# Kernel tuning notes

Hardware: AMD Instinct MI355X
Metric: run time of the kernel (lower is better)

Reference implementation:

```python
import jax, jax.numpy as jnp
import numpy as np

B, S, HID = 2, 2048, 2048
N_HEADS = 16
HEAD_DIM = HID // N_HEADS  # 128
ROPE_THETA = 10000.0
MAX_SEQ = 4096


def _rope_cache(position_ids, head_dim, theta=ROPE_THETA, max_seq=MAX_SEQ):
    # standard RoPE cache: cos/sin of shape [B, S, head_dim//2]
    half = head_dim // 2
    inv_freq = 1.0 / theta ** (jnp.arange(half, dtype=jnp.float32) / half)
    t = jnp.arange(max_seq, dtype=jnp.float32)
    freqs = jnp.outer(t, inv_freq)                      # [max_seq, half]
    pos = jnp.clip(position_ids, 0, max_seq - 1)
    return jnp.cos(freqs)[pos], jnp.sin(freqs)[pos]     # [B, S, half]


def _apply_rope(q, k, cos, sin):
    # q,k: [B, H, S, D]; cos/sin: [B, S, D/2] -> [B, 1, S, D/2]
    cos = cos[:, None, :, :]
    sin = sin[:, None, :, :]
    q1, q2 = jnp.split(q, 2, axis=-1)
    k1, k2 = jnp.split(k, 2, axis=-1)
    q_rot = jnp.concatenate([q1 * cos - q2 * sin, q2 * cos + q1 * sin], axis=-1)
    k_rot = jnp.concatenate([k1 * cos - k2 * sin, k2 * cos + k1 * sin], axis=-1)
    return q_rot, k_rot


def setup_inputs() -> dict:
    key = jax.random.key(0)
    ks = jax.random.split(key, 6)
    hidden_states = jax.random.normal(ks[0], (B, S, HID), dtype=jnp.float32)
    # additive causal mask, broadcastable over batch and heads
    causal = jnp.tril(jnp.ones((S, S), dtype=bool))
    attention_mask = jnp.where(causal, 0.0, -1e9).astype(jnp.float32)[None, None]
    position_ids = jnp.broadcast_to(jnp.arange(S, dtype=jnp.int32)[None, :], (B, S))
    scale = 0.02
    Wq = jax.random.normal(ks[1], (HID, N_HEADS * HEAD_DIM), dtype=jnp.float32) * scale
    Wk = jax.random.normal(ks[2], (HID, N_HEADS * HEAD_DIM), dtype=jnp.float32) * scale
    Wv = jax.random.normal(ks[3], (HID, N_HEADS * HEAD_DIM), dtype=jnp.float32) * scale
    Wo = jax.random.normal(ks[4], (N_HEADS * HEAD_DIM, HID), dtype=jnp.float32) * scale
    zeros = jnp.zeros((HID,), dtype=jnp.float32)
    return {
        "hidden_states": hidden_states,
        "attention_mask": attention_mask,
        "position_ids": position_ids,
        "Wq": Wq, "bq": zeros,
        "Wk": Wk, "bk": zeros,
        "Wv": Wv, "bv": zeros,
        "Wo": Wo, "bo": zeros,
    }


def reference(hidden_states, attention_mask, position_ids,
              Wq, bq, Wk, bk, Wv, bv, Wo, bo):
    b, s, _ = hidden_states.shape
    q = (hidden_states @ Wq + bq).reshape(b, s, N_HEADS, HEAD_DIM).transpose(0, 2, 1, 3)
    k = (hidden_states @ Wk + bk).reshape(b, s, N_HEADS, HEAD_DIM).transpose(0, 2, 1, 3)
    v = (hidden_states @ Wv + bv).reshape(b, s, N_HEADS, HEAD_DIM).transpose(0, 2, 1, 3)

    cos, sin = _rope_cache(position_ids, HEAD_DIM)
    q, k = _apply_rope(q, k, cos, sin)

    scores = jnp.einsum("bhqd,bhkd->bhqk", q, k) / jnp.sqrt(jnp.float32(HEAD_DIM))
    scores = scores + attention_mask
    weights = jax.nn.softmax(scores, axis=-1)
    attn = jnp.einsum("bhqk,bhkd->bhqd", weights, v)  # [B,H,S,D]
    attn = attn.transpose(0, 2, 1, 3).reshape(b, s, N_HEADS * HEAD_DIM)
    return attn @ Wo + bo
```

## Files before the change

kernel.cpp:

```cpp
#include <hip/hip_runtime.h>
#include <hip/hip_bf16.h>

typedef __bf16 bf16;
typedef bf16 bf16x4 __attribute__((ext_vector_type(4)));
typedef bf16 bf16x8 __attribute__((ext_vector_type(8)));
typedef float f32x4 __attribute__((ext_vector_type(4)));

#define B_ 2
#define S_ 2048
#define HID_ 2048
#define NH_ 16
#define HD_ 128
#define M_TOT (B_ * S_)
#define RSCALE 0.08838834764831845f
#define LN10000_OVER_64 0.14391156f

#define OFF_XB   0ull
#define OFF_WQT  (OFF_XB  + (size_t)M_TOT*HID_*2)
#define OFF_WKT  (OFF_WQT + (size_t)HID_*HID_*2)
#define OFF_WVT  (OFF_WKT + (size_t)HID_*HID_*2)
#define OFF_WOT  (OFF_WVT + (size_t)HID_*HID_*2)
#define OFF_QB   (OFF_WOT + (size_t)HID_*HID_*2)
#define OFF_KB   (OFF_QB  + (size_t)M_TOT*HID_*2)
#define OFF_VTB  (OFF_KB  + (size_t)M_TOT*HID_*2)
#define OFF_AB   (OFF_VTB + (size_t)M_TOT*HID_*2)

__device__ __forceinline__ void gload16(const bf16* g, bf16* l) {
    typedef const __attribute__((address_space(1))) unsigned int gu32;
    typedef __attribute__((address_space(3))) unsigned int lu32;
    __builtin_amdgcn_global_load_lds((gu32*)g, (lu32*)l, 16, 0, 0);
}

__global__ __launch_bounds__(256) void cvt_x(const float* __restrict__ x,
                                             bf16* __restrict__ o) {
    size_t i = ((size_t)blockIdx.x * 256 + threadIdx.x) * 4;
    float4 v = *(const float4*)(x + i);
    bf16x4 r; r[0] = (bf16)v.x; r[1] = (bf16)v.y; r[2] = (bf16)v.z; r[3] = (bf16)v.w;
    *(bf16x4*)(o + i) = r;
}

__global__ __launch_bounds__(256) void trans_w(const float* w0, const float* w1,
                                               const float* w2, const float* w3,
                                               bf16* o0, bf16* o1, bf16* o2, bf16* o3) {
    const float* W; bf16* O;
    switch (blockIdx.z) {
        case 0: W = w0; O = o0; break;
        case 1: W = w1; O = o1; break;
        case 2: W = w2; O = o2; break;
        default: W = w3; O = o3; break;
    }
    __shared__ float t[64][65];
    int tid = threadIdx.x;
    int nt0 = blockIdx.x * 64, kt0 = blockIdx.y * 64;
    #pragma unroll
    for (int p = 0; p < 4; ++p) {
        int r = p * 16 + (tid >> 4);
        int c = (tid & 15) * 4;
        float4 v = *(const float4*)(W + (size_t)(kt0 + r) * HID_ + nt0 + c);
        t[r][c + 0] = v.x; t[r][c + 1] = v.y; t[r][c + 2] = v.z; t[r][c + 3] = v.w;
    }
    __syncthreads();
    #pragma unroll
    for (int p = 0; p < 4; ++p) {
        int rr = p * 16 + (tid >> 4);
        int cc = (tid & 15) * 4;
        bf16x4 v;
        v[0] = (bf16)t[cc + 0][rr]; v[1] = (bf16)t[cc + 1][rr];
        v[2] = (bf16)t[cc + 2][rr]; v[3] = (bf16)t[cc + 3][rr];
        *(bf16x4*)(O + (size_t)(nt0 + rr) * HID_ + kt0 + cc) = v;
    }
}

__global__ __launch_bounds__(256) void gemm_qkv(const bf16* __restrict__ A,
                                                const bf16* __restrict__ Wt3,
                                                const float* __restrict__ bq,
                                                const float* __restrict__ bk,
                                                const float* __restrict__ bv,
                                                const int* __restrict__ pos_ids,
                                                bf16* __restrict__ out3) {
    __shared__ bf16 Al[128][64];
    __shared__ bf16 Bl[128][64];
    const int tid = threadIdx.x;
    const int l = tid & 63, w = tid >> 6;
    const int ln = l & 15, lg = l >> 4;
    const int bm = blockIdx.y;
    const int sel = blockIdx.x >> 4, bnn = blockIdx.x & 15;
    const bf16* Bt = Wt3 + (size_t)sel * HID_ * HID_ + (size_t)bnn * 128 * HID_;
    const float* bias = sel == 0 ? bq : (sel == 1 ? bk : bv);
    const int swz = (ln & 7) * 8;

    f32x4 acc[2][8] = {};

    for (int k0 = 0; k0 < HID_; k0 += 64) {
        __syncthreads();
        #pragma unroll
        for (int j = 0; j < 4; ++j) {
            int r0 = w * 32 + j * 8;
            int r = r0 + (l >> 3);
            int c = (((l & 7) ^ ((l >> 3) & 7))) * 8;
            gload16(A  + (size_t)(bm * 128 + r) * HID_ + k0 + c, &Al[r0][0]);
            gload16(Bt + (size_t)r * HID_ + k0 + c, &Bl[r0][0]);
        }
        __syncthreads();
        #pragma unroll
        for (int kk = 0; kk < 2; ++kk) {
            bf16x8 af[2], bfv[8];
            #pragma unroll
            for (int fm = 0; fm < 2; ++fm)
                af[fm] = *(const bf16x8*)&Al[w * 32 + fm * 16 + ln][(kk * 32 + lg * 8) ^ swz];
            #pragma unroll
            for (int fn = 0; fn < 8; ++fn)
                bfv[fn] = *(const bf16x8*)&Bl[fn * 16 + ln][(kk * 32 + lg * 8) ^ swz];
            #pragma unroll
            for (int fm = 0; fm < 2; ++fm)
                #pragma unroll
                for (int fn = 0; fn < 8; ++fn)
                    acc[fm][fn] = __builtin_amdgcn_mfma_f32_16x16x32_bf16(
                        af[fm], bfv[fn], acc[fm][fn], 0, 0, 0);
        }
    }

    #pragma unroll
    for (int fm = 0; fm < 2; ++fm) {
        #pragma unroll
        for (int i = 0; i < 4; ++i) {
            int m_g = bm * 128 + w * 32 + fm * 16 + lg * 4 + i;
            int b = m_g >> 11, s = m_g & (S_ - 1);
            if (sel == 2) {
                bf16* O = out3 + 2 * (size_t)M_TOT * HID_;
                #pragma unroll
                for (int fn = 0; fn < 8; ++fn) {
                    int d = fn * 16 + ln;
                    float v = acc[fm][fn][i] + bias[bnn * 128 + d];
                    O[((size_t)(b * NH_ + bnn) * HD_ + d) * S_ + s] = (bf16)v;
                }
            } else {
                int pos = pos_ids[m_g];
                pos = pos < 0 ? 0 : (pos > 4095 ? 4095 : pos);
                size_t base = ((size_t)(b * NH_ + bnn) * S_ + s) * HD_;
                bf16* O = out3 + (size_t)sel * M_TOT * HID_;
                #pragma unroll
                for (int fn = 0; fn < 4; ++fn) {
                    int j = fn * 16 + ln;
                    float x1 = acc[fm][fn][i]     + bias[bnn * 128 + j];
                    float x2 = acc[fm][fn + 4][i] + bias[bnn * 128 + j + 64];
                    float invf = __expf(-(float)j * LN10000_OVER_64);
                    float ang = (float)pos * invf;
                    float sn, cs;
                    __sincosf(ang, &sn, &cs);
                    float y1 = x1 * cs - x2 * sn;
                    float y2 = x2 * cs + x1 * sn;
                    if (sel == 0) { y1 *= RSCALE; y2 *= RSCALE; }
                    O[base + j]      = (bf16)y1;
                    O[base + j + 64] = (bf16)y2;
                }
            }
        }
    }
}

__global__ __launch_bounds__(256) void gemm_o(const bf16* __restrict__ A,
                                              const bf16* __restrict__ Bt,
                                              const float* __restrict__ bias,
                                              float* __restrict__ out) {
    __shared__ bf16 Al[128][64];
    __shared__ bf16 Bl[128][64];
    const int tid = threadIdx.x;
    const int l = tid & 63, w = tid >> 6;
    const int ln = l & 15, lg = l >> 4;
    const int bm = blockIdx.y, bn = blockIdx.x;
    const int swz = (ln & 7) * 8;

    f32x4 acc[2][8] = {};

    for (int k0 = 0; k0 < HID_; k0 += 64) {
        __syncthreads();
        #pragma unroll
        for (int j = 0; j < 4; ++j) {
            int r0 = w * 32 + j * 8;
            int r = r0 + (l >> 3);
            int c = (((l & 7) ^ ((l >> 3) & 7))) * 8;
            gload16(A  + (size_t)(bm * 128 + r) * HID_ + k0 + c, &Al[r0][0]);
            gload16(Bt + (size_t)(bn * 128 + r) * HID_ + k0 + c, &Bl[r0][0]);
        }
        __syncthreads();
        #pragma unroll
        for (int kk = 0; kk < 2; ++kk) {
            bf16x8 af[2], bfv[8];
            #pragma unroll
            for (int fm = 0; fm < 2; ++fm)
                af[fm] = *(const bf16x8*)&Al[w * 32 + fm * 16 + ln][(kk * 32 + lg * 8) ^ swz];
            #pragma unroll
            for (int fn = 0; fn < 8; ++fn)
                bfv[fn] = *(const bf16x8*)&Bl[fn * 16 + ln][(kk * 32 + lg * 8) ^ swz];
            #pragma unroll
            for (int fm = 0; fm < 2; ++fm)
                #pragma unroll
                for (int fn = 0; fn < 8; ++fn)
                    acc[fm][fn] = __builtin_amdgcn_mfma_f32_16x16x32_bf16(
                        af[fm], bfv[fn], acc[fm][fn], 0, 0, 0);
        }
    }

    #pragma unroll
    for (int fm = 0; fm < 2; ++fm)
        #pragma unroll
        for (int i = 0; i < 4; ++i) {
            int m_g = bm * 128 + w * 32 + fm * 16 + lg * 4 + i;
            #pragma unroll
            for (int fn = 0; fn < 8; ++fn) {
                int n_g = bn * 128 + fn * 16 + ln;
                out[(size_t)m_g * HID_ + n_g] = acc[fm][fn][i] + bias[n_g];
            }
        }
}

__global__ __launch_bounds__(512) void attn_k(const bf16* __restrict__ Q,
                                              const bf16* __restrict__ K,
                                              const bf16* __restrict__ Vt,
                                              bf16* __restrict__ O) {
    __shared__ bf16 Kl[64][136];
    __shared__ bf16 Vl[128][72];
    __shared__ bf16 Pl[8][16][72];
    const int tid = threadIdx.x;
    const int l = tid & 63, w = tid >> 6;
    const int ln = l & 15, lg = l >> 4;
    const int bid = blockIdx.x;
    const int j  = 15 - (bid >> 5);
    const int bh = bid & 31;
    const int nkt = 2 * j + 2;

    const bf16* Qb = Q  + (size_t)bh * S_ * HD_;
    const bf16* Kb = K  + (size_t)bh * S_ * HD_;
    const bf16* Vb = Vt + (size_t)bh * S_ * HD_;
    const int b = bh >> 4, h = bh & (NH_ - 1);

    const int qrow = j * 128 + w * 16 + ln;
    const int qg0  = j * 128 + w * 16 + lg * 4;

    bf16x8 qf[4];
    #pragma unroll
    for (int kk = 0; kk < 4; ++kk)
        qf[kk] = *(const bf16x8*)(Qb + (size_t)qrow * HD_ + kk * 32 + lg * 8);

    float m_run[4], l_run[4];
    #pragma unroll
    for (int i = 0; i < 4; ++i) { m_run[i] = -1e30f; l_run[i] = 0.f; }
    f32x4 oacc[8] = {};

    uint4 kr[2], vr[2];
    #pragma unroll
    for (int m = 0; m < 2; ++m) {
        int f = m * 512 + tid;
        kr[m] = *(const uint4*)(Kb + (size_t)(f >> 4) * HD_ + (f & 15) * 8);
        vr[m] = *(const uint4*)(Vb + (size_t)(f >> 3) * S_ + (f & 7) * 8);
    }

    for (int kt = 0; kt < nkt; ++kt) {
        __syncthreads();
        #pragma unroll
        for (int m = 0; m < 2; ++m) {
            int f = m * 512 + tid;
            *(uint4*)&Kl[f >> 4][(f & 15) * 8] = kr[m];
            *(uint4*)&Vl[f >> 3][(f & 7) * 8] = vr[m];
        }
        __syncthreads();
        if (kt + 1 < nkt) {
            #pragma unroll
            for (int m = 0; m < 2; ++m) {
                int f = m * 512 + tid;
                kr[m] = *(const uint4*)(Kb + (size_t)((kt + 1) * 64 + (f >> 4)) * HD_ + (f & 15) * 8);
                vr[m] = *(const uint4*)(Vb + (size_t)(f >> 3) * S_ + (kt + 1) * 64 + (f & 7) * 8);
            }
        }

        f32x4 sacc[4] = {};
        #pragma unroll
        for (int kk = 0; kk < 4; ++kk) {
            bf16x8 kf[4];
            #pragma unroll
            for (int n = 0; n < 4; ++n)
                kf[n] = *(const bf16x8*)&Kl[n * 16 + ln][kk * 32 + lg * 8];
            #pragma unroll
            for (int n = 0; n < 4; ++n)
                sacc[n] = __builtin_amdgcn_mfma_f32_16x16x32_bf16(qf[kk], kf[n], sacc[n], 0, 0, 0);
        }

        if (kt >= 2 * j) {
            #pragma unroll
            for (int n = 0; n < 4; ++n)
                #pragma unroll
                for (int i = 0; i < 4; ++i) {
                    int kg = kt * 64 + n * 16 + ln;
                    if (kg > qg0 + i) sacc[n][i] = -1e30f;
                }
        }

        float mt[4];
        #pragma unroll
        for (int i = 0; i < 4; ++i) {
            mt[i] = fmaxf(fmaxf(sacc[0][i], sacc[1][i]), fmaxf(sacc[2][i], sacc[3][i]));
            #pragma unroll
            for (int d = 1; d < 16; d <<= 1)
                mt[i] = fmaxf(mt[i], __shfl_xor(mt[i], d));
        }
        float scale[4], rs[4];
        #pragma unroll
        for (int i = 0; i < 4; ++i) {
            float mnew = fmaxf(m_run[i], mt[i]);
            scale[i] = __expf(m_run[i] - mnew);
            m_run[i] = mnew;
            rs[i] = 0.f;
        }
        #pragma unroll
        for (int n = 0; n < 4; ++n)
            #pragma unroll
            for (int i = 0; i < 4; ++i) {
                float p = __expf(sacc[n][i] - m_run[i]);
                sacc[n][i] = p;
                rs[i] += p;
            }
        #pragma unroll
        for (int i = 0; i < 4; ++i) {
            #pragma unroll
            for (int d = 1; d < 16; d <<= 1)
                rs[i] += __shfl_xor(rs[i], d);
            l_run[i] = l_run[i] * scale[i] + rs[i];
        }
        #pragma unroll
        for (int dn = 0; dn < 8; ++dn)
            #pragma unroll
            for (int i = 0; i < 4; ++i)
                oacc[dn][i] *= scale[i];

        #pragma unroll
        for (int n = 0; n < 4; ++n)
            #pragma unroll
            for (int i = 0; i < 4; ++i)
                Pl[w][lg * 4 + i][n * 16 + ln] = (bf16)sacc[n][i];

        #pragma unroll
        for (int kk = 0; kk < 2; ++kk) {
            bf16x8 pf = *(const bf16x8*)&Pl[w][ln][kk * 32 + lg * 8];
            #pragma unroll
            for (int dn = 0; dn < 8; ++dn) {
                bf16x8 vf = *(const bf16x8*)&Vl[dn * 16 + ln][kk * 32 + lg * 8];
                oacc[dn] = __builtin_amdgcn_mfma_f32_16x16x32_bf16(pf, vf, oacc[dn], 0, 0, 0);
            }
        }
    }

    #pragma unroll
    for (int i = 0; i < 4; ++i) {
        float inv = 1.0f / l_run[i];
        int s = j * 128 + w * 16 + lg * 4 + i;
        #pragma unroll
        for (int dn = 0; dn < 8; ++dn) {
            int d = dn * 16 + ln;
            O[((size_t)(b * S_ + s)) * HID_ + h * HD_ + d] = (bf16)(oacc[dn][i] * inv);
        }
    }
}

extern "C" void kernel_launch(void* const* d_in, const int* in_sizes, int n_in,
                              void* d_out, int out_size, void* d_ws, size_t ws_size,
                              hipStream_t stream) {
    const float* X    = (const float*)d_in[0];
    const int*   pos  = (const int*)d_in[2];
    const float* Wq   = (const float*)d_in[3];
    const float* bq   = (const float*)d_in[4];
    const float* Wk   = (const float*)d_in[5];
    const float* bk   = (const float*)d_in[6];
    const float* Wv   = (const float*)d_in[7];
    const float* bv   = (const float*)d_in[8];
    const float* Wo   = (const float*)d_in[9];
    const float* bo   = (const float*)d_in[10];
    float* Out = (float*)d_out;

    char* ws = (char*)d_ws;
    bf16* Xb  = (bf16*)(ws + OFF_XB);
    bf16* Wqt = (bf16*)(ws + OFF_WQT);
    bf16* Wkt = (bf16*)(ws + OFF_WKT);
    bf16* Wvt = (bf16*)(ws + OFF_WVT);
    bf16* Wot = (bf16*)(ws + OFF_WOT);
    bf16* Qb  = (bf16*)(ws + OFF_QB);
    bf16* Kb  = (bf16*)(ws + OFF_KB);
    bf16* Vtb = (bf16*)(ws + OFF_VTB);
    bf16* Ab  = (bf16*)(ws + OFF_AB);

    cvt_x<<<(M_TOT * HID_) / (256 * 4), 256, 0, stream>>>(X, Xb);
    trans_w<<<dim3(32, 32, 4), 256, 0, stream>>>(Wq, Wk, Wv, Wo, Wqt, Wkt, Wvt, Wot);

    gemm_qkv<<<dim3(48, M_TOT / 128), 256, 0, stream>>>(Xb, Wqt, bq, bk, bv, pos, Qb);

    attn_k<<<dim3(512), 512, 0, stream>>>(Qb, Kb, Vtb, Ab);

    gemm_o<<<dim3(HID_ / 128, M_TOT / 128), 256, 0, stream>>>(Ab, Wot, bo, Out);
}
```

Measured before the change: 366.7 us.

## Double-buffer attention K/V tiles in LDS with XOR swizzle and setprio

The attention kernel now keeps two LDS buffers for K and V, stores the next tile into the alternate buffer while computing on the current one, and prefetches two tiles ahead into registers, which cuts one barrier per iteration. Padded LDS rows are replaced by XOR-swizzled layouts for K, V and P to avoid bank conflicts without the padding. It also raises wave priority around the MFMA blocks and moves the P store earlier. LDS use grows because of the double buffers, which may lower occupancy, and the P buffer written before the reductions relies on per-wave ownership to avoid a race.

```diff
diff --git a/kernel.cpp b/kernel.cpp
--- a/kernel.cpp
+++ b/kernel.cpp
@@ -219,9 +219,9 @@
                                               const bf16* __restrict__ K,
                                               const bf16* __restrict__ Vt,
                                               bf16* __restrict__ O) {
-    __shared__ bf16 Kl[64][136];
-    __shared__ bf16 Vl[128][72];
-    __shared__ bf16 Pl[8][16][72];
+    __shared__ bf16 Kl[2][64][128];
+    __shared__ bf16 Vl[2][128][64];
+    __shared__ bf16 Pl[8][16][64];
     const int tid = threadIdx.x;
     const int l = tid & 63, w = tid >> 6;
     const int ln = l & 15, lg = l >> 4;
@@ -237,6 +237,8 @@
 
     const int qrow = j * 128 + w * 16 + ln;
     const int qg0  = j * 128 + w * 16 + lg * 4;
+    const int fK = tid, rK = fK >> 4, cK = fK & 15;
+    const int swzP = (ln & 7) * 8;
 
     bf16x8 qf[4];
     #pragma unroll
@@ -255,36 +257,58 @@
         kr[m] = *(const uint4*)(Kb + (size_t)(f >> 4) * HD_ + (f & 15) * 8);
         vr[m] = *(const uint4*)(Vb + (size_t)(f >> 3) * S_ + (f & 7) * 8);
     }
-
-    for (int kt = 0; kt < nkt; ++kt) {
-        __syncthreads();
+    #pragma unroll
+    for (int m = 0; m < 2; ++m) {
+        int f = m * 512 + tid;
+        int r = f >> 4,  c = f & 15;
+        int rv = f >> 3, cv = f & 7;
+        *(uint4*)&Kl[0][r][(c ^ (r & 7)) * 8] = kr[m];
+        *(uint4*)&Vl[0][rv][(cv ^ (rv & 7)) * 8] = vr[m];
+    }
+    if (nkt > 1) {
         #pragma unroll
         for (int m = 0; m < 2; ++m) {
             int f = m * 512 + tid;
-            *(uint4*)&Kl[f >> 4][(f & 15) * 8] = kr[m];
-            *(uint4*)&Vl[f >> 3][(f & 7) * 8] = vr[m];
-        }
-        __syncthreads();
+            kr[m] = *(const uint4*)(Kb + (size_t)(64 + (f >> 4)) * HD_ + (f & 15) * 8);
+            vr[m] = *(const uint4*)(Vb + (size_t)(f >> 3) * S_ + 64 + (f & 7) * 8);
+        }
+    }
+    __syncthreads();
+
+    for (int kt = 0; kt < nkt; ++kt) {
+        const int cur = kt & 1;
         if (kt + 1 < nkt) {
             #pragma unroll
             for (int m = 0; m < 2; ++m) {
                 int f = m * 512 + tid;
-                kr[m] = *(const uint4*)(Kb + (size_t)((kt + 1) * 64 + (f >> 4)) * HD_ + (f & 15) * 8);
-                vr[m] = *(const uint4*)(Vb + (size_t)(f >> 3) * S_ + (kt + 1) * 64 + (f & 7) * 8);
+                int r = f >> 4,  c = f & 15;
+                int rv = f >> 3, cv = f & 7;
+                *(uint4*)&Kl[cur ^ 1][r][(c ^ (r & 7)) * 8] = kr[m];
+                *(uint4*)&Vl[cur ^ 1][rv][(cv ^ (rv & 7)) * 8] = vr[m];
+            }
+        }
+        if (kt + 2 < nkt) {
+            #pragma unroll
+            for (int m = 0; m < 2; ++m) {
+                int f = m * 512 + tid;
+                kr[m] = *(const uint4*)(Kb + (size_t)((kt + 2) * 64 + (f >> 4)) * HD_ + (f & 15) * 8);
+                vr[m] = *(const uint4*)(Vb + (size_t)(f >> 3) * S_ + (kt + 2) * 64 + (f & 7) * 8);
             }
         }
 
         f32x4 sacc[4] = {};
+        __builtin_amdgcn_s_setprio(1);
         #pragma unroll
         for (int kk = 0; kk < 4; ++kk) {
             bf16x8 kf[4];
             #pragma unroll
             for (int n = 0; n < 4; ++n)
-                kf[n] = *(const bf16x8*)&Kl[n * 16 + ln][kk * 32 + lg * 8];
+                kf[n] = *(const bf16x8*)&Kl[cur][n * 16 + ln][(kk * 32 + lg * 8) ^ swzP];
             #pragma unroll
             for (int n = 0; n < 4; ++n)
                 sacc[n] = __builtin_amdgcn_mfma_f32_16x16x32_bf16(qf[kk], kf[n], sacc[n], 0, 0, 0);
         }
+        __builtin_amdgcn_s_setprio(0);
 
         if (kt >= 2 * j) {
             #pragma unroll
@@ -321,6 +345,12 @@
                 rs[i] += p;
             }
         #pragma unroll
+        for (int n = 0; n < 4; ++n)
+            #pragma unroll
+            for (int i = 0; i < 4; ++i)
+                Pl[w][lg * 4 + i][(n * 16 + ln) ^ (((lg * 4 + i) & 7) * 8)] = (bf16)sacc[n][i];
+
+        #pragma unroll
         for (int i = 0; i < 4; ++i) {
             #pragma unroll
             for (int d = 1; d < 16; d <<= 1)
@@ -333,21 +363,19 @@
             for (int i = 0; i < 4; ++i)
                 oacc[dn][i] *= scale[i];
 
-        #pragma unroll
-        for (int n = 0; n < 4; ++n)
-            #pragma unroll
-            for (int i = 0; i < 4; ++i)
-                Pl[w][lg * 4 + i][n * 16 + ln] = (bf16)sacc[n][i];
-
+        __builtin_amdgcn_s_setprio(1);
         #pragma unroll
         for (int kk = 0; kk < 2; ++kk) {
-            bf16x8 pf = *(const bf16x8*)&Pl[w][ln][kk * 32 + lg * 8];
+            bf16x8 pf = *(const bf16x8*)&Pl[w][ln][(kk * 32 + lg * 8) ^ swzP];
             #pragma unroll
             for (int dn = 0; dn < 8; ++dn) {
-                bf16x8 vf = *(const bf16x8*)&Vl[dn * 16 + ln][kk * 32 + lg * 8];
+                bf16x8 vf = *(const bf16x8*)&Vl[cur][dn * 16 + ln][(kk * 32 + lg * 8) ^ swzP];
                 oacc[dn] = __builtin_amdgcn_mfma_f32_16x16x32_bf16(pf, vf, oacc[dn], 0, 0, 0);
             }
         }
+        __builtin_amdgcn_s_setprio(0);
+
+        __syncthreads();
     }
 
     #pragma unroll
```

New measurement: 344.0 us. 1.07x faster.
